# Optimization experiments

Hardware: AMD Instinct MI355X
Metric: run time of the kernel (lower is better)

Reference implementation:

```python
import jax, jax.numpy as jnp
import numpy as np

B = 32768   # batch
D0 = 64     # node-0 feature dim
D1 = 64     # node-1 feature dim
M = 8       # modules per node
H = 256     # hidden width
O0 = 128    # node-0 output width
O1 = 32     # final output width
B_INIT = 0.1
INIT_W = 0.003


def _fanin_uniform(key, shape):
    bound = 1.0 / np.sqrt(shape[-2])
    return jax.random.uniform(key, shape, jnp.float32, -bound, bound)


def setup_inputs() -> dict:
    key = jax.random.key(0)
    ks = jax.random.split(key, 10)
    feat = jax.random.normal(ks[0], (B, D0 + D1), jnp.float32)
    a0 = jax.random.randint(ks[1], (B,), 0, M)
    a1 = jax.random.randint(ks[2], (B,), 0, M)
    oh0 = jax.nn.one_hot(a0, M, dtype=jnp.float32)
    oh1 = jax.nn.one_hot(a1, M, dtype=jnp.float32)
    input_val = jnp.concatenate([feat, oh0, oh1], axis=1)  # [B, 144]
    # node 0 (all post-interface, hidden init + ReLU on both layers since graph_depth < last)
    W00 = _fanin_uniform(ks[3], (M, D0, H)); b00 = jnp.full((M, H), B_INIT, jnp.float32)
    W01 = _fanin_uniform(ks[4], (M, H, O0)); b01 = jnp.full((M, O0), B_INIT, jnp.float32)
    # node 1 pre-interface (layer i=0)
    W1p = _fanin_uniform(ks[5], (M, D1, H)); b1p = jnp.full((M, H), B_INIT, jnp.float32)
    # node 1 post-interface layer i=1: input = node0_out (128) concat pre (256) = 384
    W1a = _fanin_uniform(ks[6], (M, O0 + H, O0)); b1a = jnp.full((M, O0), B_INIT, jnp.float32)
    # node 1 output layer i=2: uniform(-init_w, init_w), Identity activation
    W1o = jax.random.uniform(ks[7], (M, O0, O1), jnp.float32, -INIT_W, INIT_W)
    b1o = jax.random.uniform(ks[8], (M, O1), jnp.float32, -INIT_W, INIT_W)
    return {"input_val": input_val, "W00": W00, "b00": b00, "W01": W01, "b01": b01,
            "W1p": W1p, "b1p": b1p, "W1a": W1a, "b1a": b1a, "W1o": W1o, "b1o": b1o}


def _routed(x, W, b, onehot, act):
    # per-module linear for all modules, then one-hot select the assigned module per sample
    y = jnp.einsum('bi,mio->bmo', x, W) + b          # [B, M, out]
    y = jnp.einsum('bmo,bm->bo', y, onehot)           # [B, out]
    return jax.nn.relu(y) if act else y


def reference(input_val, W00, b00, W01, b01, W1p, b1p, W1a, b1a, W1o, b1o):
    feat0 = input_val[:, :D0]
    feat1 = input_val[:, D0:D0 + D1]
    oh0 = input_val[:, D0 + D1:D0 + D1 + M]
    oh1 = input_val[:, D0 + D1 + M:D0 + D1 + 2 * M]
    # graph depth 0, node 0: post-interface MLP (ReLU on both layers)
    h = _routed(feat0, W00, b00, oh0, True)
    h = _routed(h, W01, b01, oh0, True)               # [B, O0]
    # graph depth 1, node 1: pre-interface, concat prev-depth output, post-interface
    g = _routed(feat1, W1p, b1p, oh1, True)           # [B, H]
    g = _routed(jnp.concatenate([h, g], axis=-1), W1a, b1a, oh1, True)  # [B, O0]
    out = _routed(g, W1o, b1o, oh1, False)            # [B, O1], Identity output activation
    return out
```

## Files before the change

### kernel.cpp

```cpp
#include <hip/hip_runtime.h>
#include <hip/hip_bf16.h>

#define BATCH 32768
#define NPAIR 64
#define NBLK  128

typedef __bf16 bf16x8 __attribute__((ext_vector_type(8)));
typedef float  f32x4  __attribute__((ext_vector_type(4)));
typedef float  f32x4e __attribute__((ext_vector_type(4)));
static_assert(sizeof(bf16x8) == 16, "bf16x8 must be 16B");

#define WS_CNT      0
#define WS_BASE     256
#define WS_BH       1024
#define WS_PAIR     66560
#define WS_ROWLIST  197632
#define WS_WF00     336896
#define WS_WF01     599040
#define WS_WF1P     1123328
#define WS_WF1A     1385472
#define WS_WF1O     2171904

__device__ __forceinline__ unsigned short f2bf(float x) {
  __bf16 h = (__bf16)x;
  return __builtin_bit_cast(unsigned short, h);
}

#define KEEP(x) asm volatile("" : "+v"(x))

__global__ __launch_bounds__(256) void k_combo(const float* __restrict__ w00,
                                               const float* __restrict__ w01,
                                               const float* __restrict__ w1p,
                                               const float* __restrict__ w1a,
                                               const float* __restrict__ w1o,
                                               const float* __restrict__ inp,
                                               char* __restrict__ ws) {
  __shared__ unsigned short lds[64 * 72];
  int bid = blockIdx.x;
  if (bid >= 240) {
    int* h = (int*)lds;
    int rbid = bid - 240;
    int t = threadIdx.x;
    if (t < NPAIR) h[t] = 0;
    __syncthreads();
    int r = rbid * 256 + t;
    const float* q = inp + (size_t)r * 144 + 128;
    float4 u0 = *(const float4*)(q + 0);
    float4 u1 = *(const float4*)(q + 4);
    float4 v0 = *(const float4*)(q + 8);
    float4 v1 = *(const float4*)(q + 12);
    int a0 = 0;
    if (u0.y > 0.5f) a0 = 1; if (u0.z > 0.5f) a0 = 2; if (u0.w > 0.5f) a0 = 3;
    if (u1.x > 0.5f) a0 = 4; if (u1.y > 0.5f) a0 = 5; if (u1.z > 0.5f) a0 = 6; if (u1.w > 0.5f) a0 = 7;
    int a1 = 0;
    if (v0.y > 0.5f) a1 = 1; if (v0.z > 0.5f) a1 = 2; if (v0.w > 0.5f) a1 = 3;
    if (v1.x > 0.5f) a1 = 4; if (v1.y > 0.5f) a1 = 5; if (v1.z > 0.5f) a1 = 6; if (v1.w > 0.5f) a1 = 7;
    int p = a0 * 8 + a1;
    ((int*)(ws + WS_PAIR))[r] = p;
    atomicAdd(&h[p], 1);
    __syncthreads();
    if (t < NPAIR) ((int*)(ws + WS_BH))[rbid * NPAIR + t] = h[t];
    return;
  }
  const float* src; char* dst; int I, O, lt, NT, KC;
  if (bid < 32)       { src = w00; dst = ws + WS_WF00; I = 64;  O = 256; lt = bid;       NT = 16; KC = 2; }
  else if (bid < 96)  { src = w01; dst = ws + WS_WF01; I = 256; O = 128; lt = bid - 32;  NT = 8;  KC = 8; }
  else if (bid < 128) { src = w1p; dst = ws + WS_WF1P; I = 64;  O = 256; lt = bid - 96;  NT = 16; KC = 2; }
  else if (bid < 224) { src = w1a; dst = ws + WS_WF1A; I = 384; O = 128; lt = bid - 128; NT = 8;  KC = 12; }
  else                { src = w1o; dst = ws + WS_WF1O; I = 128; O = 32;  lt = bid - 224; NT = 2;  KC = 4; }
  int tI = I >> 6;
  int tO = (O + 63) >> 6;
  int m   = lt / (tI * tO);
  int rem = lt % (tI * tO);
  int ib = rem / tO, ob = rem % tO;
  int tx = threadIdx.x & 63, ty = threadIdx.x >> 6;
  const float* s = src + (size_t)m * I * O;
  #pragma unroll 4
  for (int s4 = 0; s4 < 16; ++s4) {
    int li = s4 * 4 + ty;
    int o  = ob * 64 + tx;
    float v = (o < O) ? s[(size_t)(ib * 64 + li) * O + o] : 0.f;
    lds[li * 72 + tx] = f2bf(v);
  }
  __syncthreads();
  int lane = threadIdx.x & 63, u = threadIdx.x >> 6;
  int ln = lane & 15, lq = lane >> 4;
  #pragma unroll
  for (int it = 0; it < 2; ++it) {
    int fi  = it * 4 + u;
    int ntl = fi >> 1, kcl = fi & 1;
    int ntg = ob * 4 + ntl, kcg = ib * 2 + kcl;
    if (ntg * 16 < O) {
      bf16x8 f;
      #pragma unroll
      for (int j = 0; j < 8; ++j)
        f[j] = __builtin_bit_cast(__bf16, lds[(kcl * 32 + lq * 8 + j) * 72 + ntl * 16 + ln]);
      *(bf16x8*)(dst + (((size_t)(m * NT + ntg) * KC + kcg) * 64 + lane) * 16) = f;
    }
  }
}

__global__ __launch_bounds__(256) void k_part(const int* __restrict__ bh,
                                              const int* __restrict__ pairArr,
                                              int* __restrict__ cnt,
                                              int* __restrict__ base,
                                              int* __restrict__ rowlist) {
  __shared__ int lbh[NBLK * NPAIR];
  __shared__ int loff[NPAIR];
  __shared__ int h[NPAIR];
  int tid = threadIdx.x, bid = blockIdx.x;
  const int4* s4 = (const int4*)bh;
  int4* d4 = (int4*)lbh;
  #pragma unroll
  for (int i = 0; i < 8; ++i) d4[tid + i * 256] = s4[tid + i * 256];
  if (tid < NPAIR) h[tid] = 0;
  __syncthreads();
  if (tid < NPAIR) {
    int c = 0, partial = 0;
    for (int b = 0; b < NBLK; ++b) {
      int v = lbh[b * NPAIR + tid];
      if (b < bid) partial += v;
      c += v;
    }
    int ntp = (c + 31) >> 5;
    int z = ntp;
    #pragma unroll
    for (int d = 1; d < 64; d <<= 1) { int y = __shfl_up(z, d); if (tid >= d) z += y; }
    int pbase = (z - ntp) * 32;
    loff[tid] = pbase + partial;
    if (bid == 0) { cnt[tid] = c; base[tid] = pbase; }
  }
  __syncthreads();
  int r = bid * 256 + tid;
  int p = pairArr[r];
  int rank = atomicAdd(&h[p], 1);
  rowlist[loff[p] + rank] = r;
}

__global__ __launch_bounds__(512, 1) void k_fused(
    const float* __restrict__ inp,
    const float* __restrict__ b00, const float* __restrict__ b01,
    const float* __restrict__ b1p, const float* __restrict__ b1a,
    const float* __restrict__ b1o,
    const char* __restrict__ ws, float* __restrict__ out)
{
  __shared__ char smem[155648];
  unsigned short* G   = (unsigned short*)(smem + 98304);
  unsigned short* H1m = (unsigned short*)(smem + 114688);
  unsigned short* HO  = (unsigned short*)(smem + 131072);
  unsigned short* G2  = (unsigned short*)(smem + 139264);
  char*           xs  = smem + 147456;

  int p     = blockIdx.x >> 2;
  int slice = blockIdx.x & 3;
  int e0 = p >> 3, e1 = p & 7;
  int cnt = ((const int*)(ws + WS_CNT))[p];
  int pbase = ((const int*)(ws + WS_BASE))[p];
  int ntp = (cnt + 31) >> 5;
  if (slice >= ntp) return;
  const int* rlbase = (const int*)(ws + WS_ROWLIST) + pbase;

  int tid  = threadIdx.x;
  {
    const f32x4e* s1 = (const f32x4e*)(ws + WS_WF1A + (size_t)e1 * 98304);
    f32x4e* d1 = (f32x4e*)smem;
    #pragma unroll
    for (int i = 0; i < 12; ++i) d1[tid + i * 512] = s1[tid + i * 512];
  }

  int lane = tid & 63;
  int w    = tid >> 6;
  int ln = lane & 15, lq = lane >> 4;
  int kcol = lq * 8;

  bf16x8 w00f[2][2], w1pf[2][2];
  #pragma unroll
  for (int nt = 0; nt < 2; ++nt)
    #pragma unroll
    for (int kc = 0; kc < 2; ++kc) {
      w00f[nt][kc] = *(const bf16x8*)(ws + WS_WF00 + (size_t)e0 * 32768 +
                                      ((((w * 2 + nt) * 2 + kc) * 64 + lane) << 4));
      w1pf[nt][kc] = *(const bf16x8*)(ws + WS_WF1P + (size_t)e1 * 32768 +
                                      ((((w * 2 + nt) * 2 + kc) * 64 + lane) << 4));
    }
  bf16x8 wc[8];
  #pragma unroll
  for (int kc = 0; kc < 8; ++kc)
    wc[kc] = *(const bf16x8*)(ws + WS_WF01 + (size_t)e0 * 65536 +
                              (((w * 8 + kc) * 64 + lane) << 4));
  #pragma unroll
  for (int nt = 0; nt < 2; ++nt)
    #pragma unroll
    for (int kc = 0; kc < 2; ++kc) { KEEP(w00f[nt][kc]); KEEP(w1pf[nt][kc]); }
  #pragma unroll
  for (int kc = 0; kc < 8; ++kc) KEEP(wc[kc]);

  float bias00[2], bias1p[2];
  #pragma unroll
  for (int nt = 0; nt < 2; ++nt) {
    bias00[nt] = b00[e0 * 256 + w * 32 + nt * 16 + ln];
    bias1p[nt] = b1p[e1 * 256 + w * 32 + nt * 16 + ln];
  }
  float bias01 = b01[e0 * 128 + w * 16 + ln];
  float bias1a = b1a[e1 * 128 + w * 16 + ln];
  float bias1o = (w < 4) ? b1o[e1 * 32 + (w >> 1) * 16 + ln] : 0.f;

  const f32x4 z4 = {0.f, 0.f, 0.f, 0.f};
  int srow = tid >> 5, scol = tid & 31;

  {
    int nr0 = min(32, cnt - slice * 32);
    const int* rl0 = rlbase + slice * 32;
    #pragma unroll
    for (int pass = 0; pass < 2; ++pass) {
      int row = pass * 16 + srow;
      int rg = (row < nr0) ? rl0[row] : -1;
      ushort4 v8 = {0, 0, 0, 0};
      if (rg >= 0) {
        f32x4e u = __builtin_nontemporal_load(
            (const f32x4e*)(inp + (size_t)rg * 144 + scol * 4));
        v8.x = f2bf(u.x); v8.y = f2bf(u.y); v8.z = f2bf(u.z); v8.w = f2bf(u.w);
      }
      int byte = (row * 256 + scol * 8) ^ ((row & 7) << 4);
      *(ushort4*)(xs + byte) = v8;
    }
  }
  __syncthreads();

  for (int t = slice; t < ntp; t += 4) {
    int nr = min(32, cnt - t * 32);
    const int* rl = rlbase + t * 32;

    int t2 = t + 4;
    bool hasNext = (t2 < ntp);
    f32x4e pre[2];
    #pragma unroll
    for (int pass = 0; pass < 2; ++pass) { pre[pass].x = 0; pre[pass].y = 0; pre[pass].z = 0; pre[pass].w = 0; }
    if (hasNext) {
      int nr2 = min(32, cnt - t2 * 32);
      const int* rl2 = rlbase + t2 * 32;
      #pragma unroll
      for (int pass = 0; pass < 2; ++pass) {
        int row = pass * 16 + srow;
        int rg = (row < nr2) ? rl2[row] : -1;
        if (rg >= 0)
          pre[pass] = __builtin_nontemporal_load(
              (const f32x4e*)(inp + (size_t)rg * 144 + scol * 4));
      }
      KEEP(pre[0]); KEEP(pre[1]);
    }

    bf16x8 axf[2][2][2];
    #pragma unroll
    for (int half = 0; half < 2; ++half)
      #pragma unroll
      for (int mt = 0; mt < 2; ++mt)
        #pragma unroll
        for (int kc = 0; kc < 2; ++kc) {
          int row = mt * 16 + ln;
          int byte = (row * 256 + half * 128 + kc * 64 + lq * 16) ^ ((row & 7) << 4);
          axf[half][mt][kc] = *(const bf16x8*)(xs + byte);
        }
    #pragma unroll
    for (int nt = 0; nt < 2; ++nt) {
      int n = w * 32 + nt * 16 + ln;
      f32x4 acc0[2] = {z4, z4}, acc1[2] = {z4, z4};
      #pragma unroll
      for (int kc = 0; kc < 2; ++kc)
        #pragma unroll
        for (int mt = 0; mt < 2; ++mt) {
          acc0[mt] = __builtin_amdgcn_mfma_f32_16x16x32_bf16(axf[0][mt][kc], w00f[nt][kc], acc0[mt], 0, 0, 0);
          acc1[mt] = __builtin_amdgcn_mfma_f32_16x16x32_bf16(axf[1][mt][kc], w1pf[nt][kc], acc1[mt], 0, 0, 0);
        }
      #pragma unroll
      for (int mt = 0; mt < 2; ++mt)
        #pragma unroll
        for (int r = 0; r < 4; ++r) {
          int row = mt * 16 + lq * 4 + r;
          int sw = ((n << 1) ^ ((row & 7) << 4));
          H1m[(row * 512 + sw) >> 1] = f2bf(fmaxf(acc0[mt][r] + bias00[nt], 0.f));
          G  [(row * 512 + sw) >> 1] = f2bf(fmaxf(acc1[mt][r] + bias1p[nt], 0.f));
        }
    }
    __syncthreads();

    if (hasNext) {
      #pragma unroll
      for (int pass = 0; pass < 2; ++pass) {
        int row = pass * 16 + srow;
        ushort4 v8;
        v8.x = f2bf(pre[pass].x); v8.y = f2bf(pre[pass].y);
        v8.z = f2bf(pre[pass].z); v8.w = f2bf(pre[pass].w);
        int byte = (row * 256 + scol * 8) ^ ((row & 7) << 4);
        *(ushort4*)(xs + byte) = v8;
      }
    }

    {
      f32x4 acc[2] = {z4, z4};
      #pragma unroll
      for (int kc = 0; kc < 8; ++kc) {
        #pragma unroll
        for (int mt = 0; mt < 2; ++mt) {
          int row = mt * 16 + ln;
          bf16x8 afr = *(const bf16x8*)&H1m[(row * 512 + (((kc * 32 + kcol) << 1) ^ ((row & 7) << 4))) >> 1];
          acc[mt] = __builtin_amdgcn_mfma_f32_16x16x32_bf16(afr, wc[kc], acc[mt], 0, 0, 0);
        }
      }
      int n = w * 16 + ln;
      #pragma unroll
      for (int mt = 0; mt < 2; ++mt)
        #pragma unroll
        for (int r = 0; r < 4; ++r) {
          int row = mt * 16 + lq * 4 + r;
          float v = fmaxf(acc[mt][r] + bias01, 0.f);
          HO[(row * 256 + ((n << 1) ^ ((row & 7) << 4))) >> 1] = f2bf(v);
        }
    }
    __syncthreads();

    {
      f32x4 acc1a[2] = {z4, z4};
      #pragma unroll
      for (int kc = 0; kc < 12; ++kc) {
        bf16x8 bfr = *(const bf16x8*)(smem + (((w * 12 + kc) * 64 + lane) << 4));
        #pragma unroll
        for (int mt = 0; mt < 2; ++mt) {
          bf16x8 afr;
          int row = mt * 16 + ln;
          if (kc < 4)
            afr = *(const bf16x8*)&HO[(row * 256 + (((kc * 32 + kcol) << 1) ^ ((row & 7) << 4))) >> 1];
          else {
            int kk = kc - 4;
            afr = *(const bf16x8*)&G[(row * 512 + (((kk * 32 + kcol) << 1) ^ ((row & 7) << 4))) >> 1];
          }
          acc1a[mt] = __builtin_amdgcn_mfma_f32_16x16x32_bf16(afr, bfr, acc1a[mt], 0, 0, 0);
        }
      }
      int n = w * 16 + ln;
      #pragma unroll
      for (int mt = 0; mt < 2; ++mt)
        #pragma unroll
        for (int r = 0; r < 4; ++r) {
          int row = mt * 16 + lq * 4 + r;
          float v = fmaxf(acc1a[mt][r] + bias1a, 0.f);
          G2[(row * 256 + ((n << 1) ^ ((row & 7) << 4))) >> 1] = f2bf(v);
        }
    }
    __syncthreads();

    if (w < 4) {
      int mt = w & 1;
      int n  = (w >> 1) * 16 + ln;
      f32x4 acc = z4;
      #pragma unroll
      for (int kc = 0; kc < 4; ++kc) {
        int row = mt * 16 + ln;
        bf16x8 afr = *(const bf16x8*)&G2[(row * 256 + (((kc * 32 + kcol) << 1) ^ ((row & 7) << 4))) >> 1];
        bf16x8 bfr = *(const bf16x8*)(ws + WS_WF1O + (size_t)e1 * 8192 +
                                      ((((w >> 1) * 4 + kc) * 64 + lane) << 4));
        acc = __builtin_amdgcn_mfma_f32_16x16x32_bf16(afr, bfr, acc, 0, 0, 0);
      }
      #pragma unroll
      for (int r = 0; r < 4; ++r) {
        int row = mt * 16 + lq * 4 + r;
        if (row < nr) {
          int rg = rl[row];
          __builtin_nontemporal_store(acc[r] + bias1o, &out[(size_t)rg * 32 + n]);
        }
      }
    }
  }
}

extern "C" void kernel_launch(void* const* d_in, const int* in_sizes, int n_in,
                              void* d_out, int out_size, void* d_ws, size_t ws_size,
                              hipStream_t stream) {
  const float* inp = (const float*)d_in[0];
  const float* w00 = (const float*)d_in[1];
  const float* b00 = (const float*)d_in[2];
  const float* w01 = (const float*)d_in[3];
  const float* b01 = (const float*)d_in[4];
  const float* w1p = (const float*)d_in[5];
  const float* b1p = (const float*)d_in[6];
  const float* w1a = (const float*)d_in[7];
  const float* b1a = (const float*)d_in[8];
  const float* w1o = (const float*)d_in[9];
  const float* b1o = (const float*)d_in[10];
  char*  ws  = (char*)d_ws;
  float* out = (float*)d_out;

  k_combo<<<368, 256, 0, stream>>>(w00, w01, w1p, w1a, w1o, inp, ws);
  k_part<<<NBLK, 256, 0, stream>>>((const int*)(ws + WS_BH),
                                   (const int*)(ws + WS_PAIR),
                                   (int*)(ws + WS_CNT), (int*)(ws + WS_BASE),
                                   (int*)(ws + WS_ROWLIST));
  k_fused<<<256, 512, 0, stream>>>(inp, b00, b01, b1p, b1a, b1o, ws, out);
}
```

Baseline: 45.30 us.

## Double row tile to 64 and split W1a between LDS and registers

Each block now processes 64-row tiles instead of 32, doubling the M dimension of every MFMA stage, so the staged per-expert weights are reused across more rows and fewer tiles and barriers are needed per pair. To make room in LDS for the larger activation buffers, only the first 5 K-chunks of W1a are staged in shared memory and the remaining 7 are kept in registers. The final-layer weights are preloaded into registers, and all 8 waves now take part in the output layer. The cost is higher register pressure, fewer tiles per pair (less parallelism when counts are small), and the 4-slice split leaving some blocks idle.

```diff
diff --git a/kernel.cpp b/kernel.cpp
--- a/kernel.cpp
+++ b/kernel.cpp
@@ -145,18 +145,18 @@
     const char* __restrict__ ws, float* __restrict__ out)
 {
   __shared__ char smem[155648];
-  unsigned short* G   = (unsigned short*)(smem + 98304);
-  unsigned short* H1m = (unsigned short*)(smem + 114688);
-  unsigned short* HO  = (unsigned short*)(smem + 131072);
-  unsigned short* G2  = (unsigned short*)(smem + 139264);
-  char*           xs  = smem + 147456;
+  unsigned short* G   = (unsigned short*)(smem + 40960);
+  unsigned short* H1m = (unsigned short*)(smem + 73728);
+  unsigned short* HO  = (unsigned short*)(smem + 106496);
+  unsigned short* G2  = (unsigned short*)(smem + 122880);
+  char*           xs  = smem + 139264;
 
   int p     = blockIdx.x >> 2;
   int slice = blockIdx.x & 3;
   int e0 = p >> 3, e1 = p & 7;
   int cnt = ((const int*)(ws + WS_CNT))[p];
   int pbase = ((const int*)(ws + WS_BASE))[p];
-  int ntp = (cnt + 31) >> 5;
+  int ntp = (cnt + 63) >> 6;
   if (slice >= ntp) return;
   const int* rlbase = (const int*)(ws + WS_ROWLIST) + pbase;
 
@@ -165,7 +165,12 @@
     const f32x4e* s1 = (const f32x4e*)(ws + WS_WF1A + (size_t)e1 * 98304);
     f32x4e* d1 = (f32x4e*)smem;
     #pragma unroll
-    for (int i = 0; i < 12; ++i) d1[tid + i * 512] = s1[tid + i * 512];
+    for (int i = 0; i < 5; ++i) {
+      int fidx = tid + i * 512;
+      int chunk = fidx >> 6, within = fidx & 63;
+      int w2 = chunk / 5, kc = chunk % 5;
+      d1[fidx] = s1[(w2 * 12 + kc) * 64 + within];
+    }
   }
 
   int lane = tid & 63;
@@ -188,12 +193,29 @@
   for (int kc = 0; kc < 8; ++kc)
     wc[kc] = *(const bf16x8*)(ws + WS_WF01 + (size_t)e0 * 65536 +
                               (((w * 8 + kc) * 64 + lane) << 4));
+  bf16x8 wa_hi[7];
+  #pragma unroll
+  for (int j = 0; j < 7; ++j)
+    wa_hi[j] = *(const bf16x8*)(ws + WS_WF1A + (size_t)e1 * 98304 +
+                                (((w * 12 + 5 + j) * 64 + lane) << 4));
+  bf16x8 wo[4];
+  {
+    int nch = w & 1;
+    #pragma unroll
+    for (int kc = 0; kc < 4; ++kc)
+      wo[kc] = *(const bf16x8*)(ws + WS_WF1O + (size_t)e1 * 8192 +
+                                (((nch * 4 + kc) * 64 + lane) << 4));
+  }
   #pragma unroll
   for (int nt = 0; nt < 2; ++nt)
     #pragma unroll
     for (int kc = 0; kc < 2; ++kc) { KEEP(w00f[nt][kc]); KEEP(w1pf[nt][kc]); }
   #pragma unroll
   for (int kc = 0; kc < 8; ++kc) KEEP(wc[kc]);
+  #pragma unroll
+  for (int j = 0; j < 7; ++j) KEEP(wa_hi[j]);
+  #pragma unroll
+  for (int kc = 0; kc < 4; ++kc) KEEP(wo[kc]);
 
   float bias00[2], bias1p[2];
   #pragma unroll
@@ -203,16 +225,16 @@
   }
   float bias01 = b01[e0 * 128 + w * 16 + ln];
   float bias1a = b1a[e1 * 128 + w * 16 + ln];
-  float bias1o = (w < 4) ? b1o[e1 * 32 + (w >> 1) * 16 + ln] : 0.f;
+  float bias1o = b1o[e1 * 32 + (w & 1) * 16 + ln];
 
   const f32x4 z4 = {0.f, 0.f, 0.f, 0.f};
   int srow = tid >> 5, scol = tid & 31;
 
   {
-    int nr0 = min(32, cnt - slice * 32);
-    const int* rl0 = rlbase + slice * 32;
-    #pragma unroll
-    for (int pass = 0; pass < 2; ++pass) {
+    int nr0 = min(64, cnt - slice * 64);
+    const int* rl0 = rlbase + slice * 64;
+    #pragma unroll
+    for (int pass = 0; pass < 4; ++pass) {
       int row = pass * 16 + srow;
       int rg = (row < nr0) ? rl0[row] : -1;
       ushort4 v8 = {0, 0, 0, 0};
@@ -228,65 +250,67 @@
   __syncthreads();
 
   for (int t = slice; t < ntp; t += 4) {
-    int nr = min(32, cnt - t * 32);
-    const int* rl = rlbase + t * 32;
+    int nr = min(64, cnt - t * 64);
+    const int* rl = rlbase + t * 64;
 
     int t2 = t + 4;
     bool hasNext = (t2 < ntp);
-    f32x4e pre[2];
-    #pragma unroll
-    for (int pass = 0; pass < 2; ++pass) { pre[pass].x = 0; pre[pass].y = 0; pre[pass].z = 0; pre[pass].w = 0; }
+    f32x4e pre[4];
+    #pragma unroll
+    for (int pass = 0; pass < 4; ++pass) { pre[pass].x = 0; pre[pass].y = 0; pre[pass].z = 0; pre[pass].w = 0; }
     if (hasNext) {
-      int nr2 = min(32, cnt - t2 * 32);
-      const int* rl2 = rlbase + t2 * 32;
-      #pragma unroll
-      for (int pass = 0; pass < 2; ++pass) {
+      int nr2 = min(64, cnt - t2 * 64);
+      const int* rl2 = rlbase + t2 * 64;
+      #pragma unroll
+      for (int pass = 0; pass < 4; ++pass) {
         int row = pass * 16 + srow;
         int rg = (row < nr2) ? rl2[row] : -1;
         if (rg >= 0)
           pre[pass] = __builtin_nontemporal_load(
               (const f32x4e*)(inp + (size_t)rg * 144 + scol * 4));
       }
-      KEEP(pre[0]); KEEP(pre[1]);
-    }
-
-    bf16x8 axf[2][2][2];
-    #pragma unroll
-    for (int half = 0; half < 2; ++half)
-      #pragma unroll
-      for (int mt = 0; mt < 2; ++mt)
+      KEEP(pre[0]); KEEP(pre[1]); KEEP(pre[2]); KEEP(pre[3]);
+    }
+
+    #pragma unroll
+    for (int layer = 0; layer < 2; ++layer) {
+      bf16x8 axf[4][2];
+      #pragma unroll
+      for (int mt = 0; mt < 4; ++mt)
         #pragma unroll
         for (int kc = 0; kc < 2; ++kc) {
           int row = mt * 16 + ln;
-          int byte = (row * 256 + half * 128 + kc * 64 + lq * 16) ^ ((row & 7) << 4);
-          axf[half][mt][kc] = *(const bf16x8*)(xs + byte);
-        }
-    #pragma unroll
-    for (int nt = 0; nt < 2; ++nt) {
-      int n = w * 32 + nt * 16 + ln;
-      f32x4 acc0[2] = {z4, z4}, acc1[2] = {z4, z4};
-      #pragma unroll
-      for (int kc = 0; kc < 2; ++kc)
-        #pragma unroll
-        for (int mt = 0; mt < 2; ++mt) {
-          acc0[mt] = __builtin_amdgcn_mfma_f32_16x16x32_bf16(axf[0][mt][kc], w00f[nt][kc], acc0[mt], 0, 0, 0);
-          acc1[mt] = __builtin_amdgcn_mfma_f32_16x16x32_bf16(axf[1][mt][kc], w1pf[nt][kc], acc1[mt], 0, 0, 0);
-        }
-      #pragma unroll
-      for (int mt = 0; mt < 2; ++mt)
-        #pragma unroll
-        for (int r = 0; r < 4; ++r) {
-          int row = mt * 16 + lq * 4 + r;
-          int sw = ((n << 1) ^ ((row & 7) << 4));
-          H1m[(row * 512 + sw) >> 1] = f2bf(fmaxf(acc0[mt][r] + bias00[nt], 0.f));
-          G  [(row * 512 + sw) >> 1] = f2bf(fmaxf(acc1[mt][r] + bias1p[nt], 0.f));
-        }
+          int byte = (row * 256 + layer * 128 + kc * 64 + lq * 16) ^ ((row & 7) << 4);
+          axf[mt][kc] = *(const bf16x8*)(xs + byte);
+        }
+      unsigned short* dst = layer ? G : H1m;
+      #pragma unroll
+      for (int nt = 0; nt < 2; ++nt) {
+        int n = w * 32 + nt * 16 + ln;
+        float bs = layer ? bias1p[nt] : bias00[nt];
+        f32x4 acc[4] = {z4, z4, z4, z4};
+        #pragma unroll
+        for (int kc = 0; kc < 2; ++kc) {
+          bf16x8 bfr = layer ? w1pf[nt][kc] : w00f[nt][kc];
+          #pragma unroll
+          for (int mt = 0; mt < 4; ++mt)
+            acc[mt] = __builtin_amdgcn_mfma_f32_16x16x32_bf16(axf[mt][kc], bfr, acc[mt], 0, 0, 0);
+        }
+        #pragma unroll
+        for (int mt = 0; mt < 4; ++mt)
+          #pragma unroll
+          for (int r = 0; r < 4; ++r) {
+            int row = mt * 16 + lq * 4 + r;
+            float v = fmaxf(acc[mt][r] + bs, 0.f);
+            dst[(row * 512 + ((n << 1) ^ ((row & 7) << 4))) >> 1] = f2bf(v);
+          }
+      }
     }
     __syncthreads();
 
     if (hasNext) {
       #pragma unroll
-      for (int pass = 0; pass < 2; ++pass) {
+      for (int pass = 0; pass < 4; ++pass) {
         int row = pass * 16 + srow;
         ushort4 v8;
         v8.x = f2bf(pre[pass].x); v8.y = f2bf(pre[pass].y);
@@ -297,11 +321,11 @@
     }
 
     {
-      f32x4 acc[2] = {z4, z4};
+      f32x4 acc[4] = {z4, z4, z4, z4};
       #pragma unroll
       for (int kc = 0; kc < 8; ++kc) {
         #pragma unroll
-        for (int mt = 0; mt < 2; ++mt) {
+        for (int mt = 0; mt < 4; ++mt) {
           int row = mt * 16 + ln;
           bf16x8 afr = *(const bf16x8*)&H1m[(row * 512 + (((kc * 32 + kcol) << 1) ^ ((row & 7) << 4))) >> 1];
           acc[mt] = __builtin_amdgcn_mfma_f32_16x16x32_bf16(afr, wc[kc], acc[mt], 0, 0, 0);
@@ -309,7 +333,7 @@
       }
       int n = w * 16 + ln;
       #pragma unroll
-      for (int mt = 0; mt < 2; ++mt)
+      for (int mt = 0; mt < 4; ++mt)
         #pragma unroll
         for (int r = 0; r < 4; ++r) {
           int row = mt * 16 + lq * 4 + r;
@@ -320,12 +344,14 @@
     __syncthreads();
 
     {
-      f32x4 acc1a[2] = {z4, z4};
+      f32x4 acc1a[4] = {z4, z4, z4, z4};
       #pragma unroll
       for (int kc = 0; kc < 12; ++kc) {
-        bf16x8 bfr = *(const bf16x8*)(smem + (((w * 12 + kc) * 64 + lane) << 4));
-        #pragma unroll
-        for (int mt = 0; mt < 2; ++mt) {
+        bf16x8 bfr = (kc < 5)
+          ? *(const bf16x8*)(smem + (((w * 5 + kc) * 64 + lane) << 4))
+          : wa_hi[kc - 5];
+        #pragma unroll
+        for (int mt = 0; mt < 4; ++mt) {
           bf16x8 afr;
           int row = mt * 16 + ln;
           if (kc < 4)
@@ -339,7 +365,7 @@
       }
       int n = w * 16 + ln;
       #pragma unroll
-      for (int mt = 0; mt < 2; ++mt)
+      for (int mt = 0; mt < 4; ++mt)
         #pragma unroll
         for (int r = 0; r < 4; ++r) {
           int row = mt * 16 + lq * 4 + r;
@@ -349,17 +375,15 @@
     }
     __syncthreads();
 
-    if (w < 4) {
-      int mt = w & 1;
-      int n  = (w >> 1) * 16 + ln;
+    {
+      int mt  = w >> 1;
+      int n   = (w & 1) * 16 + ln;
       f32x4 acc = z4;
       #pragma unroll
       for (int kc = 0; kc < 4; ++kc) {
         int row = mt * 16 + ln;
         bf16x8 afr = *(const bf16x8*)&G2[(row * 256 + (((kc * 32 + kcol) << 1) ^ ((row & 7) << 4))) >> 1];
-        bf16x8 bfr = *(const bf16x8*)(ws + WS_WF1O + (size_t)e1 * 8192 +
-                                      ((((w >> 1) * 4 + kc) * 64 + lane) << 4));
-        acc = __builtin_amdgcn_mfma_f32_16x16x32_bf16(afr, bfr, acc, 0, 0, 0);
+        acc = __builtin_amdgcn_mfma_f32_16x16x32_bf16(afr, wo[kc], acc, 0, 0, 0);
       }
       #pragma unroll
       for (int r = 0; r < 4; ++r) {
```

Result: slower. 87.46 us (+93.0%).
